# Performance work log

Hardware: AMD Instinct MI355X
Metric: run time of the kernel (lower is better)

The kernel has to match this reference:

```python
import jax, jax.numpy as jnp
import numpy as np

B, N_ROIS, C, H, W = 4, 180, 512, 48, 48
STRIDE = 4
EPS = 1e-5


def _pool_one(feat, roi):
    # feat: [C,H,W], roi: [4] float (y1,x1,y2,x2) in image coords
    r = roi / STRIDE
    r0 = jnp.trunc(r[0]).astype(jnp.int32)
    r1 = jnp.trunc(r[1]).astype(jnp.int32)
    r2 = jnp.ceil(r[2]).astype(jnp.int32)
    r3 = jnp.ceil(r[3]).astype(jnp.int32)
    h_size = r2 - r0 + 1
    w_size = r3 - r1 + 1
    idx2 = jnp.arange(2)
    # AdaptiveMaxPool2d region boundaries: [floor(i*s/2), ceil((i+1)*s/2))
    sh = (idx2 * h_size) // 2
    eh = ((idx2 + 1) * h_size + 1) // 2
    sw = (idx2 * w_size) // 2
    ew = ((idx2 + 1) * w_size + 1) // 2
    hh = jnp.arange(H)[None, :]
    ww = jnp.arange(W)[None, :]
    mask_h = (hh >= (r0 + sh)[:, None]) & (hh < (r0 + eh)[:, None])  # [2,H]
    mask_w = (ww >= (r1 + sw)[:, None]) & (ww < (r1 + ew)[:, None])  # [2,W]
    neg = jnp.finfo(feat.dtype).min
    # max over W within each col region -> [2(oj), C, H]
    mw = jnp.where(mask_w[:, None, None, :], feat[None], neg).max(axis=-1)
    # max over H within each row region -> [2(oi), 2(oj), C]
    p = jnp.where(mask_h[:, None, None, :], mw[None], neg).max(axis=-1)
    # torch layout: [C, oi, oj] then flatten row-major
    return jnp.transpose(p, (2, 0, 1)).reshape(-1)  # [C*4]


def _roi_pool(features, rois):
    # features: [B,C,H,W], rois: [B,N,4] -> [B,N,C*4]
    def per_roi(roi_b):  # roi_b: [B,4]
        return jax.vmap(_pool_one)(features, roi_b)  # [B, C*4]
    out = jax.lax.map(per_roi, jnp.swapaxes(rois, 0, 1))  # [N,B,C*4]
    return jnp.swapaxes(out, 0, 1)


def _bn(x, gamma, beta):
    # training-mode BatchNorm1d over [B, N_ROIS(channels), F]: stats over (B,F)
    mean = x.mean(axis=(0, 2), keepdims=True)
    var = ((x - mean) ** 2).mean(axis=(0, 2), keepdims=True)
    return (x - mean) * jax.lax.rsqrt(var + EPS) * gamma[None, :, None] + beta[None, :, None]


def setup_inputs() -> dict:
    key = jax.random.key(0)
    k1, k2, k3, k4, k5 = jax.random.split(key, 5)
    features = jax.random.normal(k1, (B, C, H, W), dtype=jnp.float32)
    max_coord = (H - 1) * STRIDE
    y = jnp.sort(jax.random.uniform(k2, (B, N_ROIS, 2), minval=0.0, maxval=max_coord), axis=-1)
    x = jnp.sort(jax.random.uniform(k3, (B, N_ROIS, 2), minval=0.0, maxval=max_coord), axis=-1)
    rois = jnp.stack([y[..., 0], x[..., 0], y[..., 1], x[..., 1]], axis=-1)  # [B,N,4]
    F_in = C * 4
    W1 = jax.random.normal(k4, (64, F_in), dtype=jnp.float32) * 0.02
    bl1 = jnp.zeros((64,), dtype=jnp.float32)
    gamma1 = jnp.ones((N_ROIS,), dtype=jnp.float32)
    beta1 = jnp.zeros((N_ROIS,), dtype=jnp.float32)
    gamma2 = jnp.ones((N_ROIS,), dtype=jnp.float32)
    beta2 = jnp.zeros((N_ROIS,), dtype=jnp.float32)
    return {"features": features, "rois": rois, "gamma1": gamma1, "beta1": beta1,
            "W1": W1, "bl1": bl1, "gamma2": gamma2, "beta2": beta2}


def reference(features, rois, gamma1, beta1, W1, bl1, gamma2, beta2):
    pooled = _roi_pool(features, rois)            # [B, 180, 2048]
    x = jax.nn.relu(pooled)
    x = _bn(x, gamma1, beta1)
    y = jnp.einsum('bnf,of->bno', x, W1) + bl1    # [B, 180, 64]
    y = _bn(y, gamma2, beta2)
    return y
```

## Files before the change

### kernel.cpp

```cpp
#include <hip/hip_runtime.h>
#include <hip/hip_bf16.h>
#include <cfloat>
#include <math.h>

#define BB 4
#define NR 180
#define CC 512
#define HH 48
#define WW 48
#define FF (CC*4)
#define OO 64
#define EPSV 1e-5f
#define NCH 4


typedef unsigned short us2 __attribute__((ext_vector_type(2)));

__device__ __forceinline__ unsigned pmax(unsigned a, unsigned b) {
    return __builtin_bit_cast(unsigned, __builtin_elementwise_max(
        __builtin_bit_cast(us2, a), __builtin_bit_cast(us2, b)));
}
__device__ __forceinline__ uint4 pmax4(uint4 a, uint4 b) {
    return make_uint4(pmax(a.x,b.x), pmax(a.y,b.y), pmax(a.z,b.z), pmax(a.w,b.w));
}
__device__ __forceinline__ unsigned mapb(float f) {
    unsigned fu = __float_as_uint(f);
    unsigned u = fu >> 16;
    return (fu >> 31) ? (~u & 0xFFFFu) : (u | 0x8000u);
}
__device__ __forceinline__ void unmap2(unsigned m, float& lo, float& hi) {
    unsigned t = ((~m) >> 15) & 0x00010001u;
    unsigned u = m ^ (0x80008000u ^ (t * 0x7FFFu));
    lo = __uint_as_float(u << 16);
    hi = __uint_as_float(u & 0xffff0000u);
}

__global__ __launch_bounds__(256) void k_prep(const float* __restrict__ feat,
                                              const float* __restrict__ W1,
                                              ushort* __restrict__ featB,
                                              float* __restrict__ W1T4) {
    __shared__ float tile[32][33];
    int t = threadIdx.x;
    int z = blockIdx.z;

    if (z < 4) {
        const int S = HH * WW;
        int b  = z;
        int s0 = blockIdx.x * 32;
        int c0 = blockIdx.y * 32;
        const float* src = feat + (size_t)b * CC * S;
        ushort* dst = featB + (size_t)b * S * CC;

        int cl = t >> 3;
        int sx = (t & 7) << 2;
        float4 v = *(const float4*)(src + (size_t)(c0 + cl) * S + s0 + sx);
        tile[cl][sx] = v.x; tile[cl][sx+1] = v.y; tile[cl][sx+2] = v.z; tile[cl][sx+3] = v.w;
        __syncthreads();

        int sl = t >> 3;
        int c4 = (t & 7) << 2;
        unsigned u0 = mapb(tile[c4][sl])   | (mapb(tile[c4+1][sl]) << 16);
        unsigned u1 = mapb(tile[c4+2][sl]) | (mapb(tile[c4+3][sl]) << 16);
        *(uint2*)(dst + (size_t)(s0 + sl) * CC + c0 + c4) = make_uint2(u0, u1);
    } else {
        if (blockIdx.x >= 8) return;
        int kt = blockIdx.y * 8 + blockIdx.x;
        int k0 = (kt >> 1) * 32, o0 = (kt & 1) * 32;
        int tx = t & 31, ty = t >> 5;
        #pragma unroll
        for (int k = 0; k < 4; k++) {
            int row = ty + k * 8;
            tile[row][tx] = W1[(size_t)(o0 + row) * FF + (k0 + tx)];
        }
        __syncthreads();
        #pragma unroll
        for (int k = 0; k < 4; k++) {
            int row = ty + k * 8;
            int kk = k0 + row;
            int o  = o0 + tx;
            W1T4[(size_t)(kk >> 2) * 256 + o * 4 + (kk & 3)] = tile[tx][row];
        }
    }
}

__global__ __launch_bounds__(256, 6) void k_pool(const ushort* __restrict__ featB,
                                                 const float* __restrict__ rois,
                                                 ushort* __restrict__ pp) {
    __shared__ unsigned lu[4][16][64];
    int ch = blockIdx.x;
    int bn = blockIdx.y;
    int b = bn & 3, n = bn >> 2;
    int tid = threadIdx.x;
    int g = tid >> 6, c = tid & 63;

    const float* roi = rois + ((size_t)b * NR + n) * 4;
    int r0 = (int)(roi[0] * 0.25f);
    int r1 = (int)(roi[1] * 0.25f);
    int r2 = (int)ceilf(roi[2] * 0.25f);
    int r3 = (int)ceilf(roi[3] * 0.25f);
    int hs  = r2 - r0 + 1;
    int wsz = r3 - r1 + 1;
    int eh0 = (hs + 1) >> 1, sh1 = hs >> 1;
    int ew0 = (wsz + 1) >> 1, sw1 = wsz >> 1;

    const uint4 Z = make_uint4(0,0,0,0);
    uint4 q00 = Z, q01 = Z, q10 = Z, q11 = Z;

    for (int L = ch * 4 + g; L < hs; L += 16) {
        const uint4* rp = (const uint4*)(featB + ((size_t)((b * HH + r0 + L) * WW + r1)) * CC) + c;
        uint4 cm0 = Z, cm1 = Z;
        {
            int e = ew0 - 1;
            for (int w = 0; w < ew0; w += 8) {
                uint4 u0 = rp[(size_t)64 * w];
                uint4 u1 = rp[(size_t)64 * min(w + 1, e)];
                uint4 u2 = rp[(size_t)64 * min(w + 2, e)];
                uint4 u3 = rp[(size_t)64 * min(w + 3, e)];
                uint4 u4 = rp[(size_t)64 * min(w + 4, e)];
                uint4 u5 = rp[(size_t)64 * min(w + 5, e)];
                uint4 u6 = rp[(size_t)64 * min(w + 6, e)];
                uint4 u7 = rp[(size_t)64 * min(w + 7, e)];
                cm0 = pmax4(cm0, pmax4(pmax4(pmax4(u0,u1), pmax4(u2,u3)),
                                       pmax4(pmax4(u4,u5), pmax4(u6,u7))));
            }
        }
        {
            int e = wsz - 1;
            for (int w = sw1; w < wsz; w += 8) {
                uint4 u0 = rp[(size_t)64 * w];
                uint4 u1 = rp[(size_t)64 * min(w + 1, e)];
                uint4 u2 = rp[(size_t)64 * min(w + 2, e)];
                uint4 u3 = rp[(size_t)64 * min(w + 3, e)];
                uint4 u4 = rp[(size_t)64 * min(w + 4, e)];
                uint4 u5 = rp[(size_t)64 * min(w + 5, e)];
                uint4 u6 = rp[(size_t)64 * min(w + 6, e)];
                uint4 u7 = rp[(size_t)64 * min(w + 7, e)];
                cm1 = pmax4(cm1, pmax4(pmax4(pmax4(u0,u1), pmax4(u2,u3)),
                                       pmax4(pmax4(u4,u5), pmax4(u6,u7))));
            }
        }
        if (L <  eh0) { q00 = pmax4(q00, cm0); q01 = pmax4(q01, cm1); }
        if (L >= sh1) { q10 = pmax4(q10, cm0); q11 = pmax4(q11, cm1); }
    }

    {
        unsigned* L0 = &lu[g][0][c];
        #define REPK(mcomp, a, bq, jc0) \
            L0[((jc0)*2+0)*64]   = ((a) & 0xFFFFu) | ((bq) << 16); \
            L0[((jc0)*2+0+2)*64] = ((a) >> 16) | ((bq) & 0xFFFF0000u);
        #define REPK2(mcomp) { \
            unsigned a0 = q00.mcomp, a1 = q01.mcomp, b0 = q10.mcomp, b1 = q11.mcomp; \
            int jeven = (2*(&q00.mcomp - &q00.x)); (void)jeven; }
        #undef REPK
        #undef REPK2
        unsigned a, b2;
        a = q00.x; b2 = q01.x;
        lu[g][0*4 + 0][c] = (a & 0xFFFFu) | (b2 << 16);
        lu[g][0*4 + 2][c] = (a >> 16)     | (b2 & 0xFFFF0000u);
        a = q10.x; b2 = q11.x;
        lu[g][0*4 + 1][c] = (a & 0xFFFFu) | (b2 << 16);
        lu[g][0*4 + 3][c] = (a >> 16)     | (b2 & 0xFFFF0000u);
        a = q00.y; b2 = q01.y;
        lu[g][1*4 + 0][c] = (a & 0xFFFFu) | (b2 << 16);
        lu[g][1*4 + 2][c] = (a >> 16)     | (b2 & 0xFFFF0000u);
        a = q10.y; b2 = q11.y;
        lu[g][1*4 + 1][c] = (a & 0xFFFFu) | (b2 << 16);
        lu[g][1*4 + 3][c] = (a >> 16)     | (b2 & 0xFFFF0000u);
        a = q00.z; b2 = q01.z;
        lu[g][2*4 + 0][c] = (a & 0xFFFFu) | (b2 << 16);
        lu[g][2*4 + 2][c] = (a >> 16)     | (b2 & 0xFFFF0000u);
        a = q10.z; b2 = q11.z;
        lu[g][2*4 + 1][c] = (a & 0xFFFFu) | (b2 << 16);
        lu[g][2*4 + 3][c] = (a >> 16)     | (b2 & 0xFFFF0000u);
        a = q00.w; b2 = q01.w;
        lu[g][3*4 + 0][c] = (a & 0xFFFFu) | (b2 << 16);
        lu[g][3*4 + 2][c] = (a >> 16)     | (b2 & 0xFFFF0000u);
        a = q10.w; b2 = q11.w;
        lu[g][3*4 + 1][c] = (a & 0xFFFFu) | (b2 << 16);
        lu[g][3*4 + 3][c] = (a >> 16)     | (b2 & 0xFFFF0000u);
    }
    __syncthreads();

    int c2 = tid & 63, j0 = (tid >> 6) * 4;
    unsigned ou[4];
    #pragma unroll
    for (int jj = 0; jj < 4; jj++) {
        int j = j0 + jj;
        unsigned m = pmax(pmax(lu[0][j][c2], lu[1][j][c2]),
                          pmax(lu[2][j][c2], lu[3][j][c2]));
        ou[jj] = pmax(m, 0x80008000u);
    }
    unsigned* dst = (unsigned*)(pp + ((size_t)(b * NR + n) * NCH + ch) * FF);
    *(uint4*)(dst + c2 * 16 + j0) = make_uint4(ou[0], ou[1], ou[2], ou[3]);
}


__global__ __launch_bounds__(1024) void k_gemm(const ushort* __restrict__ pp,
                                               const float* __restrict__ W1T4,
                                               const float* __restrict__ bl1,
                                               const float* __restrict__ g1,
                                               const float* __restrict__ b1,
                                               const float* __restrict__ g2,
                                               const float* __restrict__ b2,
                                               float* __restrict__ out) {
    __shared__ float xs[BB][FF];
    __shared__ float pd[16][BB][OO];
    __shared__ float pw[16][OO];
    __shared__ float part_s[16], part_q[16];
    __shared__ float sm2[4], sq2[4];
    int n = blockIdx.x;
    int tid = threadIdx.x;

    float s_acc = 0.f, q_acc = 0.f;
    #pragma unroll
    for (int k2 = 0; k2 < 2; k2++) {
        int gi = tid + (k2 << 10);
        int bb = gi >> 9;
        int idx = gi & 511;
        const unsigned* base = (const unsigned*)(pp + ((size_t)(bb * NR + n)) * NCH * FF);
        uint2 m = *(const uint2*)(base + 0 * (FF / 2) + idx * 2);
        #pragma unroll
        for (int cch = 1; cch < NCH; cch++) {
            uint2 u = *(const uint2*)(base + cch * (FF / 2) + idx * 2);
            m.x = pmax(m.x, u.x);
            m.y = pmax(m.y, u.y);
        }
        float v0, v1, v2, v3;
        unmap2(m.x, v0, v1);
        unmap2(m.y, v2, v3);
        *(float4*)&xs[bb][idx << 2] = make_float4(v0, v1, v2, v3);
        s_acc += v0 + v1 + v2 + v3;
        q_acc += v0*v0 + v1*v1 + v2*v2 + v3*v3;
    }
    for (int off = 32; off; off >>= 1) {
        s_acc += __shfl_down(s_acc, off);
        q_acc += __shfl_down(q_acc, off);
    }
    if ((tid & 63) == 0) { part_s[tid >> 6] = s_acc; part_q[tid >> 6] = q_acc; }
    __syncthreads();
    float ts = 0.f, tq = 0.f;
    #pragma unroll
    for (int i = 0; i < 16; i++) { ts += part_s[i]; tq += part_q[i]; }
    const float inv1 = 1.f / (float)(BB * FF);
    float mean = ts * inv1;
    float var  = tq * inv1 - mean * mean;
    float a1n  = g1[n] * rsqrtf(var + EPSV);
    float c1n  = b1[n] - mean * a1n;

    int sc = tid >> 6;
    int o  = tid & 63;
    int k4a = sc << 5;
    float a0 = 0.f, a1 = 0.f, a2 = 0.f, a3 = 0.f, wsum = 0.f;
    #pragma unroll 4
    for (int k4 = k4a; k4 < k4a + 32; k4++) {
        float4 w4 = *(const float4*)(W1T4 + (size_t)k4 * 256 + o * 4);
        float4 x0 = *(const float4*)&xs[0][k4 << 2];
        float4 x1 = *(const float4*)&xs[1][k4 << 2];
        float4 x2 = *(const float4*)&xs[2][k4 << 2];
        float4 x3 = *(const float4*)&xs[3][k4 << 2];
        wsum += w4.x + w4.y + w4.z + w4.w;
        a0 += w4.x*x0.x + w4.y*x0.y + w4.z*x0.z + w4.w*x0.w;
        a1 += w4.x*x1.x + w4.y*x1.y + w4.z*x1.z + w4.w*x1.w;
        a2 += w4.x*x2.x + w4.y*x2.y + w4.z*x2.z + w4.w*x2.w;
        a3 += w4.x*x3.x + w4.y*x3.y + w4.z*x3.z + w4.w*x3.w;
    }
    pd[sc][0][o] = a0; pd[sc][1][o] = a1; pd[sc][2][o] = a2; pd[sc][3][o] = a3;
    pw[sc][o] = wsum;
    __syncthreads();

    float y = 0.f;
    int b = tid >> 6;
    if (tid < 256) {
        float dot = 0.f, wsm = 0.f;
        #pragma unroll
        for (int ss = 0; ss < 16; ss++) { dot += pd[ss][b][o]; wsm += pw[ss][o]; }
        y = a1n * dot + c1n * wsm + bl1[o];
        float rs = y, rq = y * y;
        for (int off = 32; off; off >>= 1) {
            rs += __shfl_down(rs, off);
            rq += __shfl_down(rq, off);
        }
        if (o == 0) { sm2[b] = rs; sq2[b] = rq; }
    }
    __syncthreads();
    if (tid < 256) {
        float sm  = sm2[0] + sm2[1] + sm2[2] + sm2[3];
        float sqm = sq2[0] + sq2[1] + sq2[2] + sq2[3];
        const float inv2 = 1.f / 256.f;
        float mean2 = sm * inv2;
        float var2  = sqm * inv2 - mean2 * mean2;
        float r2s = rsqrtf(var2 + EPSV);
        out[((size_t)b * NR + n) * OO + o] = (y - mean2) * r2s * g2[n] + b2[n];
    }
}

extern "C" void kernel_launch(void* const* d_in, const int* in_sizes, int n_in,
                              void* d_out, int out_size, void* d_ws, size_t ws_size,
                              hipStream_t stream) {
    const float* feat = (const float*)d_in[0];
    const float* rois = (const float*)d_in[1];
    const float* g1   = (const float*)d_in[2];
    const float* b1   = (const float*)d_in[3];
    const float* W1   = (const float*)d_in[4];
    const float* bl1  = (const float*)d_in[5];
    const float* g2   = (const float*)d_in[6];
    const float* b2   = (const float*)d_in[7];
    float* out = (float*)d_out;

    ushort* featB = (ushort*)d_ws;
    float*  W1T4  = (float*)(featB + (size_t)BB*HH*WW*CC);
    ushort* pp    = (ushort*)(W1T4 + (size_t)OO*FF);

    k_prep<<<dim3(72, 16, 5), 256, 0, stream>>>(feat, W1, featB, W1T4);
    k_pool<<<dim3(NCH, BB * NR), 256, 0, stream>>>(featB, rois, pp);
    k_gemm<<<NR, 1024, 0, stream>>>(pp, W1T4, bl1, g1, b1, g2, b2, out);
}
```

Before: 116.9 us.

## Use sparse-table row max along W and fuse pooling into GEMM kernel

Adds a kernel that builds a sparse table of power-of-two windowed maxima along the W axis for each feature row (levels 2,4,8,16). Each ROI column-region max then needs only two overlapping table lookups instead of scanning every W position. The pooling is also merged into the GEMM/BN kernel, so one block per ROI index handles all batches and the intermediate pooled buffer disappears. The cost is writing four extra feature-sized tables (more memory traffic up front), plus a pooling stage with less parallelism: 180 blocks of 1024 threads, each thread looping over rows.

```diff
diff --git a/kernel.cpp b/kernel.cpp
--- a/kernel.cpp
+++ b/kernel.cpp
@@ -11,7 +11,7 @@
 #define FF (CC*4)
 #define OO 64
 #define EPSV 1e-5f
-#define NCH 4
+#define TW_LEVEL ((size_t)BB*HH*WW*CC)
 
 
 typedef unsigned short us2 __attribute__((ext_vector_type(2)));
@@ -83,15 +83,64 @@
     }
 }
 
-__global__ __launch_bounds__(256, 6) void k_pool(const ushort* __restrict__ featB,
-                                                 const float* __restrict__ rois,
-                                                 ushort* __restrict__ pp) {
-    __shared__ unsigned lu[4][16][64];
-    int ch = blockIdx.x;
-    int bn = blockIdx.y;
-    int b = bn & 3, n = bn >> 2;
+__global__ __launch_bounds__(256) void k_tab(const ushort* __restrict__ featB,
+                                             ushort* __restrict__ Tw) {
+    __shared__ uint4 A[WW][64];
+    int by = blockIdx.x;
+    int b = by / HH, y = by % HH;
+    int t = threadIdx.x;
+    const uint4* src = (const uint4*)(featB + (size_t)((b * HH + y) * WW) * CC);
+
+    #pragma unroll
+    for (int i = 0; i < 12; i++) {
+        int it = t + i * 256;
+        A[it >> 6][it & 63] = src[it];
+    }
+    __syncthreads();
+
+    for (int k = 1; k <= 4; k++) {
+        int h = 1 << (k - 1);
+        uint4* dst = (uint4*)(Tw + ((size_t)(k - 1) * BB * HH + b * HH + y) * (size_t)(WW * CC));
+        uint4 v[12];
+        #pragma unroll
+        for (int i = 0; i < 12; i++) {
+            int it = t + i * 256;
+            int x = it >> 6, c = it & 63;
+            v[i] = pmax4(A[x][c], A[min(x + h, WW - 1)][c]);
+        }
+        __syncthreads();
+        #pragma unroll
+        for (int i = 0; i < 12; i++) {
+            int it = t + i * 256;
+            A[it >> 6][it & 63] = v[i];
+            dst[it] = v[i];
+        }
+        __syncthreads();
+    }
+}
+
+__global__ __launch_bounds__(1024) void k_pg(const ushort* __restrict__ featB,
+                                             const ushort* __restrict__ Tw,
+                                             const float* __restrict__ rois,
+                                             const float* __restrict__ W1T4,
+                                             const float* __restrict__ bl1,
+                                             const float* __restrict__ g1,
+                                             const float* __restrict__ b1,
+                                             const float* __restrict__ g2,
+                                             const float* __restrict__ b2,
+                                             float* __restrict__ out) {
+    __shared__ unsigned lu[BB][4][16][65];
+    __shared__ float xs[BB][FF];
+    __shared__ float pd[16][BB][OO];
+    __shared__ float pw[16][OO];
+    __shared__ float part_s[16], part_q[16];
+    __shared__ float sm2[4], sq2[4];
+
+    int n = blockIdx.x;
     int tid = threadIdx.x;
-    int g = tid >> 6, c = tid & 63;
+    int b  = tid >> 8;
+    int g  = (tid >> 6) & 3;
+    int c  = tid & 63;
 
     const float* roi = rois + ((size_t)b * NR + n) * 4;
     int r0 = (int)(roi[0] * 0.25f);
@@ -103,132 +152,76 @@
     int eh0 = (hs + 1) >> 1, sh1 = hs >> 1;
     int ew0 = (wsz + 1) >> 1, sw1 = wsz >> 1;
 
+    int len0 = ew0;
+    int k0 = 31 - __clz(len0);
+    int x0a = r1, x0b = r1 + len0 - (1 << k0);
+    int len1 = wsz - sw1;
+    int k1 = 31 - __clz(len1);
+    int x1a = r1 + sw1, x1b = r1 + wsz - (1 << k1);
+
+    const ushort* base0 = (k0 == 0) ? featB : (Tw + (size_t)(k0 - 1) * TW_LEVEL);
+    const ushort* base1 = (k1 == 0) ? featB : (Tw + (size_t)(k1 - 1) * TW_LEVEL);
+
     const uint4 Z = make_uint4(0,0,0,0);
     uint4 q00 = Z, q01 = Z, q10 = Z, q11 = Z;
-
-    for (int L = ch * 4 + g; L < hs; L += 16) {
-        const uint4* rp = (const uint4*)(featB + ((size_t)((b * HH + r0 + L) * WW + r1)) * CC) + c;
-        uint4 cm0 = Z, cm1 = Z;
-        {
-            int e = ew0 - 1;
-            for (int w = 0; w < ew0; w += 8) {
-                uint4 u0 = rp[(size_t)64 * w];
-                uint4 u1 = rp[(size_t)64 * min(w + 1, e)];
-                uint4 u2 = rp[(size_t)64 * min(w + 2, e)];
-                uint4 u3 = rp[(size_t)64 * min(w + 3, e)];
-                uint4 u4 = rp[(size_t)64 * min(w + 4, e)];
-                uint4 u5 = rp[(size_t)64 * min(w + 5, e)];
-                uint4 u6 = rp[(size_t)64 * min(w + 6, e)];
-                uint4 u7 = rp[(size_t)64 * min(w + 7, e)];
-                cm0 = pmax4(cm0, pmax4(pmax4(pmax4(u0,u1), pmax4(u2,u3)),
-                                       pmax4(pmax4(u4,u5), pmax4(u6,u7))));
-            }
-        }
-        {
-            int e = wsz - 1;
-            for (int w = sw1; w < wsz; w += 8) {
-                uint4 u0 = rp[(size_t)64 * w];
-                uint4 u1 = rp[(size_t)64 * min(w + 1, e)];
-                uint4 u2 = rp[(size_t)64 * min(w + 2, e)];
-                uint4 u3 = rp[(size_t)64 * min(w + 3, e)];
-                uint4 u4 = rp[(size_t)64 * min(w + 4, e)];
-                uint4 u5 = rp[(size_t)64 * min(w + 5, e)];
-                uint4 u6 = rp[(size_t)64 * min(w + 6, e)];
-                uint4 u7 = rp[(size_t)64 * min(w + 7, e)];
-                cm1 = pmax4(cm1, pmax4(pmax4(pmax4(u0,u1), pmax4(u2,u3)),
-                                       pmax4(pmax4(u4,u5), pmax4(u6,u7))));
-            }
-        }
+    for (int L = g; L < hs; L += 4) {
+        size_t rowoff = (size_t)((b * HH + r0 + L) * WW) * CC;
+        const uint4* p0 = (const uint4*)(base0 + rowoff) + c;
+        const uint4* p1 = (const uint4*)(base1 + rowoff) + c;
+        uint4 cm0 = pmax4(p0[(size_t)64 * x0a], p0[(size_t)64 * x0b]);
+        uint4 cm1 = pmax4(p1[(size_t)64 * x1a], p1[(size_t)64 * x1b]);
         if (L <  eh0) { q00 = pmax4(q00, cm0); q01 = pmax4(q01, cm1); }
         if (L >= sh1) { q10 = pmax4(q10, cm0); q11 = pmax4(q11, cm1); }
     }
 
     {
-        unsigned* L0 = &lu[g][0][c];
-        #define REPK(mcomp, a, bq, jc0) \
-            L0[((jc0)*2+0)*64]   = ((a) & 0xFFFFu) | ((bq) << 16); \
-            L0[((jc0)*2+0+2)*64] = ((a) >> 16) | ((bq) & 0xFFFF0000u);
-        #define REPK2(mcomp) { \
-            unsigned a0 = q00.mcomp, a1 = q01.mcomp, b0 = q10.mcomp, b1 = q11.mcomp; \
-            int jeven = (2*(&q00.mcomp - &q00.x)); (void)jeven; }
-        #undef REPK
-        #undef REPK2
-        unsigned a, b2;
-        a = q00.x; b2 = q01.x;
-        lu[g][0*4 + 0][c] = (a & 0xFFFFu) | (b2 << 16);
-        lu[g][0*4 + 2][c] = (a >> 16)     | (b2 & 0xFFFF0000u);
-        a = q10.x; b2 = q11.x;
-        lu[g][0*4 + 1][c] = (a & 0xFFFFu) | (b2 << 16);
-        lu[g][0*4 + 3][c] = (a >> 16)     | (b2 & 0xFFFF0000u);
-        a = q00.y; b2 = q01.y;
-        lu[g][1*4 + 0][c] = (a & 0xFFFFu) | (b2 << 16);
-        lu[g][1*4 + 2][c] = (a >> 16)     | (b2 & 0xFFFF0000u);
-        a = q10.y; b2 = q11.y;
-        lu[g][1*4 + 1][c] = (a & 0xFFFFu) | (b2 << 16);
-        lu[g][1*4 + 3][c] = (a >> 16)     | (b2 & 0xFFFF0000u);
-        a = q00.z; b2 = q01.z;
-        lu[g][2*4 + 0][c] = (a & 0xFFFFu) | (b2 << 16);
-        lu[g][2*4 + 2][c] = (a >> 16)     | (b2 & 0xFFFF0000u);
-        a = q10.z; b2 = q11.z;
-        lu[g][2*4 + 1][c] = (a & 0xFFFFu) | (b2 << 16);
-        lu[g][2*4 + 3][c] = (a >> 16)     | (b2 & 0xFFFF0000u);
-        a = q00.w; b2 = q01.w;
-        lu[g][3*4 + 0][c] = (a & 0xFFFFu) | (b2 << 16);
-        lu[g][3*4 + 2][c] = (a >> 16)     | (b2 & 0xFFFF0000u);
-        a = q10.w; b2 = q11.w;
-        lu[g][3*4 + 1][c] = (a & 0xFFFFu) | (b2 << 16);
-        lu[g][3*4 + 3][c] = (a >> 16)     | (b2 & 0xFFFF0000u);
-    }
-    __syncthreads();
-
-    int c2 = tid & 63, j0 = (tid >> 6) * 4;
-    unsigned ou[4];
+        unsigned* L0 = &lu[b][g][0][c];
+        unsigned a, p2;
+        a = q00.x; p2 = q01.x;
+        L0[ 0*65] = (a & 0xFFFFu) | (p2 << 16);
+        L0[ 2*65] = (a >> 16)     | (p2 & 0xFFFF0000u);
+        a = q10.x; p2 = q11.x;
+        L0[ 1*65] = (a & 0xFFFFu) | (p2 << 16);
+        L0[ 3*65] = (a >> 16)     | (p2 & 0xFFFF0000u);
+        a = q00.y; p2 = q01.y;
+        L0[ 4*65] = (a & 0xFFFFu) | (p2 << 16);
+        L0[ 6*65] = (a >> 16)     | (p2 & 0xFFFF0000u);
+        a = q10.y; p2 = q11.y;
+        L0[ 5*65] = (a & 0xFFFFu) | (p2 << 16);
+        L0[ 7*65] = (a >> 16)     | (p2 & 0xFFFF0000u);
+        a = q00.z; p2 = q01.z;
+        L0[ 8*65] = (a & 0xFFFFu) | (p2 << 16);
+        L0[10*65] = (a >> 16)     | (p2 & 0xFFFF0000u);
+        a = q10.z; p2 = q11.z;
+        L0[ 9*65] = (a & 0xFFFFu) | (p2 << 16);
+        L0[11*65] = (a >> 16)     | (p2 & 0xFFFF0000u);
+        a = q00.w; p2 = q01.w;
+        L0[12*65] = (a & 0xFFFFu) | (p2 << 16);
+        L0[14*65] = (a >> 16)     | (p2 & 0xFFFF0000u);
+        a = q10.w; p2 = q11.w;
+        L0[13*65] = (a & 0xFFFFu) | (p2 << 16);
+        L0[15*65] = (a >> 16)     | (p2 & 0xFFFF0000u);
+    }
+    __syncthreads();
+
+    float s_acc = 0.f, q_acc = 0.f;
+    int s  = tid & 255;
+    int bb = tid >> 8;
     #pragma unroll
-    for (int jj = 0; jj < 4; jj++) {
-        int j = j0 + jj;
-        unsigned m = pmax(pmax(lu[0][j][c2], lu[1][j][c2]),
-                          pmax(lu[2][j][c2], lu[3][j][c2]));
-        ou[jj] = pmax(m, 0x80008000u);
-    }
-    unsigned* dst = (unsigned*)(pp + ((size_t)(b * NR + n) * NCH + ch) * FF);
-    *(uint4*)(dst + c2 * 16 + j0) = make_uint4(ou[0], ou[1], ou[2], ou[3]);
-}
-
-
-__global__ __launch_bounds__(1024) void k_gemm(const ushort* __restrict__ pp,
-                                               const float* __restrict__ W1T4,
-                                               const float* __restrict__ bl1,
-                                               const float* __restrict__ g1,
-                                               const float* __restrict__ b1,
-                                               const float* __restrict__ g2,
-                                               const float* __restrict__ b2,
-                                               float* __restrict__ out) {
-    __shared__ float xs[BB][FF];
-    __shared__ float pd[16][BB][OO];
-    __shared__ float pw[16][OO];
-    __shared__ float part_s[16], part_q[16];
-    __shared__ float sm2[4], sq2[4];
-    int n = blockIdx.x;
-    int tid = threadIdx.x;
-
-    float s_acc = 0.f, q_acc = 0.f;
-    #pragma unroll
-    for (int k2 = 0; k2 < 2; k2++) {
-        int gi = tid + (k2 << 10);
-        int bb = gi >> 9;
-        int idx = gi & 511;
-        const unsigned* base = (const unsigned*)(pp + ((size_t)(bb * NR + n)) * NCH * FF);
-        uint2 m = *(const uint2*)(base + 0 * (FF / 2) + idx * 2);
-        #pragma unroll
-        for (int cch = 1; cch < NCH; cch++) {
-            uint2 u = *(const uint2*)(base + cch * (FF / 2) + idx * 2);
-            m.x = pmax(m.x, u.x);
-            m.y = pmax(m.y, u.y);
-        }
+    for (int p = 0; p < 2; p++) {
+        int fb = (p << 10) + (s << 2);
+        int cc = fb >> 5;
+        int j0 = (fb >> 1) & 15;
+        unsigned m0 = pmax(pmax(lu[bb][0][j0  ][cc], lu[bb][1][j0  ][cc]),
+                           pmax(lu[bb][2][j0  ][cc], lu[bb][3][j0  ][cc]));
+        unsigned m1 = pmax(pmax(lu[bb][0][j0+1][cc], lu[bb][1][j0+1][cc]),
+                           pmax(lu[bb][2][j0+1][cc], lu[bb][3][j0+1][cc]));
+        m0 = pmax(m0, 0x80008000u);
+        m1 = pmax(m1, 0x80008000u);
         float v0, v1, v2, v3;
-        unmap2(m.x, v0, v1);
-        unmap2(m.y, v2, v3);
-        *(float4*)&xs[bb][idx << 2] = make_float4(v0, v1, v2, v3);
+        unmap2(m0, v0, v1);
+        unmap2(m1, v2, v3);
+        *(float4*)&xs[bb][fb] = make_float4(v0, v1, v2, v3);
         s_acc += v0 + v1 + v2 + v3;
         q_acc += v0*v0 + v1*v1 + v2*v2 + v3*v3;
     }
@@ -269,18 +262,18 @@
     __syncthreads();
 
     float y = 0.f;
-    int b = tid >> 6;
+    int bo = tid >> 6;
     if (tid < 256) {
         float dot = 0.f, wsm = 0.f;
         #pragma unroll
-        for (int ss = 0; ss < 16; ss++) { dot += pd[ss][b][o]; wsm += pw[ss][o]; }
+        for (int ss = 0; ss < 16; ss++) { dot += pd[ss][bo][o]; wsm += pw[ss][o]; }
         y = a1n * dot + c1n * wsm + bl1[o];
         float rs = y, rq = y * y;
         for (int off = 32; off; off >>= 1) {
             rs += __shfl_down(rs, off);
             rq += __shfl_down(rq, off);
         }
-        if (o == 0) { sm2[b] = rs; sq2[b] = rq; }
+        if (o == 0) { sm2[bo] = rs; sq2[bo] = rq; }
     }
     __syncthreads();
     if (tid < 256) {
@@ -290,7 +283,7 @@
         float mean2 = sm * inv2;
         float var2  = sqm * inv2 - mean2 * mean2;
         float r2s = rsqrtf(var2 + EPSV);
-        out[((size_t)b * NR + n) * OO + o] = (y - mean2) * r2s * g2[n] + b2[n];
+        out[((size_t)bo * NR + n) * OO + o] = (y - mean2) * r2s * g2[n] + b2[n];
     }
 }
 
@@ -309,9 +302,9 @@
 
     ushort* featB = (ushort*)d_ws;
     float*  W1T4  = (float*)(featB + (size_t)BB*HH*WW*CC);
-    ushort* pp    = (ushort*)(W1T4 + (size_t)OO*FF);
+    ushort* Tw    = (ushort*)(W1T4 + (size_t)OO*FF);
 
     k_prep<<<dim3(72, 16, 5), 256, 0, stream>>>(feat, W1, featB, W1T4);
-    k_pool<<<dim3(NCH, BB * NR), 256, 0, stream>>>(featB, rois, pp);
-    k_gemm<<<NR, 1024, 0, stream>>>(pp, W1T4, bl1, g1, b1, g2, b2, out);
-}
+    k_tab<<<dim3(BB * HH), 256, 0, stream>>>(featB, Tw);
+    k_pg<<<dim3(NR), 1024, 0, stream>>>(featB, Tw, rois, W1T4, bl1, g1, b1, g2, b2, out);
+}
```

Result: faster. 108.0 us (-7.7%).
